# Optimization experiments

Measured on AMD Instinct MI355X. Metric: run time of the kernel, lower is better.

The kernel has to match this reference:

```python
import jax, jax.numpy as jnp
import numpy as np

B, S, D = 4, 1024, 4096
HQ, HKV = 32, 8
HD = D // HQ          # 128
SCALE = HQ // HKV     # 4 (GQA repeat factor)


def setup_inputs() -> dict:
    key = jax.random.key(0)
    ks = jax.random.split(key, 11)
    s = 0.02  # init scale for weights
    return {
        "x": jax.random.normal(ks[0], (B, S, D), jnp.float32),
        # freqs_cis stored as (real, imag) pairs: [S, HD//2, 2]
        "freqs_cis": jax.random.normal(ks[1], (S, HD // 2, 2), jnp.float32),
        "Wq": jax.random.normal(ks[2], (D, HQ * HD), jnp.float32) * s,
        "bq": jnp.zeros((HQ * HD,), jnp.float32),
        "Wk": jax.random.normal(ks[3], (D, HKV * HD), jnp.float32) * s,
        "bk": jnp.zeros((HKV * HD,), jnp.float32),
        "Wv": jax.random.normal(ks[4], (D, HKV * HD), jnp.float32) * s,
        "bv": jnp.zeros((HKV * HD,), jnp.float32),
        "Wo": jax.random.normal(ks[5], (D, D), jnp.float32) * s,
        "bo": jnp.zeros((D,), jnp.float32),
        "startpos": 0,
    }


def _apply_rotary(x, fc):
    # x: [B, S, H, HD]; fc: [S, HD//2, 2] (real, imag)
    xr = x.reshape(*x.shape[:-1], HD // 2, 2)
    a, b = xr[..., 0], xr[..., 1]
    c = fc[None, :, None, :, 0]  # [1, S, 1, HD//2]
    d = fc[None, :, None, :, 1]
    # complex multiply (a+ib)*(c+id)
    out = jnp.stack([a * c - b * d, a * d + b * c], axis=-1)
    return out.reshape(x.shape)


def reference(x, freqs_cis, Wq, bq, Wk, bk, Wv, bv, Wo, bo, startpos):
    b, s, _ = x.shape
    q = (x @ Wq + bq).reshape(b, s, HQ, HD)
    k = (x @ Wk + bk).reshape(b, s, HKV, HD)
    v = (x @ Wv + bv).reshape(b, s, HKV, HD)

    fc = freqs_cis[startpos:startpos + s]
    q = _apply_rotary(q, fc)
    k = _apply_rotary(k, fc)

    # startpos == 0 and seq == cache_seq: cache write/read is identity
    q = q.transpose(0, 2, 1, 3)                            # [b, HQ, s, HD]
    k = jnp.repeat(k.transpose(0, 2, 1, 3), SCALE, axis=1)  # GQA repeat -> [b, HQ, s, HD]
    v = jnp.repeat(v.transpose(0, 2, 1, 3), SCALE, axis=1)

    scores = jnp.einsum('bhqd,bhkd->bhqk', q, k) / jnp.sqrt(jnp.float32(HD))
    causal = jnp.tril(jnp.ones((s, s), bool))
    scores = jnp.where(causal, scores, -jnp.inf)
    attn = jax.nn.softmax(scores, axis=-1)
    o = jnp.einsum('bhqk,bhkd->bhqd', attn, v)
    o = o.transpose(0, 2, 1, 3).reshape(b, s, HQ * HD)
    return o @ Wo + bo
```

## Files before the change

### kernel.cpp

```cpp
#include <hip/hip_runtime.h>
#include <hip/hip_bf16.h>

using bf16x8   = __attribute__((ext_vector_type(8))) __bf16;
using floatx4  = __attribute__((ext_vector_type(4))) float;
using floatx16 = __attribute__((ext_vector_type(16))) float;

#define DEVINL __device__ __forceinline__

DEVINL void gload16(const void* g, void* l) {
  __builtin_amdgcn_global_load_lds(
      (__attribute__((address_space(1))) void*)g,
      (__attribute__((address_space(3))) void*)l,
      16, 0, 0);
}

constexpr int S_ = 1024, D_ = 4096, HQ_ = 32, HKV_ = 8, HD_ = 128, B_ = 4;

__global__ void conv_bf16(const float* __restrict__ in, __bf16* __restrict__ out, int n) {
  int i = (blockIdx.x * 256 + threadIdx.x) * 8;
  if (i >= n) return;
  float4 a = *(const float4*)(in + i);
  float4 b = *(const float4*)(in + i + 4);
  bf16x8 o;
  o[0] = (__bf16)a.x; o[1] = (__bf16)a.y; o[2] = (__bf16)a.z; o[3] = (__bf16)a.w;
  o[4] = (__bf16)b.x; o[5] = (__bf16)b.y; o[6] = (__bf16)b.z; o[7] = (__bf16)b.w;
  *(bf16x8*)(out + i) = o;
}

__global__ void conv_transpose(const float* __restrict__ W, __bf16* __restrict__ WT, int K, int N) {
  __shared__ float tile[32][33];
  int n0 = blockIdx.x * 32, k0 = blockIdx.y * 32;
  int tx = threadIdx.x & 31, ty = threadIdx.x >> 5;
#pragma unroll
  for (int i = 0; i < 32; i += 8)
    tile[ty + i][tx] = W[(size_t)(k0 + ty + i) * N + n0 + tx];
  __syncthreads();
#pragma unroll
  for (int i = 0; i < 32; i += 8)
    WT[(size_t)(n0 + ty + i) * K + k0 + tx] = (__bf16)tile[tx][ty + i];
}

template<int MODE>
__global__ __launch_bounds__(512, 1)
void gemm8p(const __bf16* __restrict__ A, const __bf16* __restrict__ BT,
            const float* __restrict__ b0, const float* __restrict__ b1,
            const float* __restrict__ b2, void* __restrict__ Cout,
            int M, int N, int K)
{
  __shared__ __bf16 lds[65536];
  const int t = threadIdx.x;
  const int lane = t & 63, w = t >> 6;
  const int wm = w >> 2, wn = w & 3;
  const int g = (lane >> 4) & 3, c = lane & 15;

  const int gridX = gridDim.x;
  const int nwg = gridDim.x * gridDim.y;
  int lin = blockIdx.y * gridDim.x + blockIdx.x;
  lin = (lin & 7) * (nwg >> 3) + (lin >> 3);
  const int bx = lin % gridX, by = lin / gridX;
  const int m0 = by * 256, n0 = bx * 256;

  const floatx4 zero4 = {0.f, 0.f, 0.f, 0.f};
  floatx4 acc[2][2][4][2];
#pragma unroll
  for (int a = 0; a < 2; a++)
#pragma unroll
    for (int bq = 0; bq < 2; bq++)
#pragma unroll
      for (int i = 0; i < 4; i++)
#pragma unroll
        for (int j = 0; j < 2; j++) acc[a][bq][i][j] = zero4;

  const int t3 = t >> 3;
  const int l8 = ((t & 7) ^ (t3 & 7)) * 8;
  const int browc = (t3 & 31) + ((t3 >> 5) << 6);
  const __bf16* srcA0 = A  + (size_t)(m0 + t3) * K + l8;
  const __bf16* srcA1 = A  + (size_t)(m0 + 64 + t3) * K + l8;
  const __bf16* srcB0 = BT + (size_t)(n0 + browc) * K + l8;
  const __bf16* srcB1 = BT + (size_t)(n0 + 32 + browc) * K + l8;
  const size_t k128 = (size_t)128 * K;

  const int arow_rd = (wm * 64 + c) * 64;
  const int brow_rd = (wn * 32 + c) * 64;
  const int sel0 = ((g) ^ (c & 7)) * 8;
  const int sel1 = ((4 + g) ^ (c & 7)) * 8;

  const int NT = K >> 6;

  bf16x8 af[4][2], bf0[2][2], bf1[2][2];

#define STG(srcp, subofs, kt, pbuf)                                              \
  gload16((srcp) + (size_t)(kt) * 64,        &lds[(pbuf) + (subofs) + t * 8]);   \
  gload16((srcp) + (size_t)(kt) * 64 + k128, &lds[(pbuf) + (subofs) + 4096 + t * 8]);

#define LOADA(MQ, bb)                                                            \
  _Pragma("unroll")                                                              \
  for (int i = 0; i < 4; i++) {                                                  \
    af[i][0] = *(const bf16x8*)&lds[(bb) + (MQ)*8192 + arow_rd + i*1024 + sel0]; \
    af[i][1] = *(const bf16x8*)&lds[(bb) + (MQ)*8192 + arow_rd + i*1024 + sel1]; \
  }

#define LOADB(DST, NQ, bb)                                                       \
  _Pragma("unroll")                                                              \
  for (int j = 0; j < 2; j++) {                                                  \
    DST[j][0] = *(const bf16x8*)&lds[(bb) + 16384 + (NQ)*8192 + brow_rd + j*1024 + sel0]; \
    DST[j][1] = *(const bf16x8*)&lds[(bb) + 16384 + (NQ)*8192 + brow_rd + j*1024 + sel1]; \
  }

#define MFMAQ(MQ, NQ, BF)                                                        \
  __builtin_amdgcn_s_setprio(1);                                                 \
  _Pragma("unroll")                                                              \
  for (int i = 0; i < 4; i++)                                                    \
    _Pragma("unroll")                                                            \
    for (int j = 0; j < 2; j++) {                                                \
      acc[MQ][NQ][i][j] = __builtin_amdgcn_mfma_f32_16x16x32_bf16(af[i][0], BF[j][0], acc[MQ][NQ][i][j], 0, 0, 0); \
      acc[MQ][NQ][i][j] = __builtin_amdgcn_mfma_f32_16x16x32_bf16(af[i][1], BF[j][1], acc[MQ][NQ][i][j], 0, 0, 0); \
    }                                                                            \
  __builtin_amdgcn_s_setprio(0);

#define SBAR() __builtin_amdgcn_sched_barrier(0)
#define BARR() __builtin_amdgcn_s_barrier()
#define VMC(N) asm volatile("s_waitcnt vmcnt(" #N ")" ::: "memory");
#define LGKM0() asm volatile("s_waitcnt lgkmcnt(0)" ::: "memory");

  STG(srcA0, 0, 0, 0)
  STG(srcB0, 16384, 0, 0)
  STG(srcB1, 24576, 0, 0)
  STG(srcA1, 8192, 0, 0)
  VMC(4) BARR(); SBAR();

  for (int v = 0; v < NT - 1; ++v) {
    const int bb = (v & 1) * 32768;
    const int nb = bb ^ 32768;
    LOADA(0, bb)
    LOADB(bf0, 0, bb)
    STG(srcA0, 0, v + 1, nb)
    SBAR(); VMC(4) BARR(); LGKM0() SBAR();
    MFMAQ(0, 0, bf0)
    SBAR(); BARR(); SBAR();
    LOADB(bf1, 1, bb)
    STG(srcB0, 16384, v + 1, nb)
    SBAR(); VMC(4) BARR(); LGKM0() SBAR();
    MFMAQ(0, 1, bf1)
    SBAR(); BARR(); SBAR();
    LOADA(1, bb)
    STG(srcB1, 24576, v + 1, nb)
    SBAR(); BARR(); LGKM0() SBAR();
    MFMAQ(1, 1, bf1)
    SBAR(); BARR(); SBAR();
    STG(srcA1, 8192, v + 1, nb)
    SBAR(); VMC(4) BARR(); SBAR();
    MFMAQ(1, 0, bf0)
    SBAR(); BARR(); SBAR();
  }
  {
    const int bb = ((NT - 1) & 1) * 32768;
    LOADA(0, bb)
    LOADB(bf0, 0, bb)
    SBAR(); VMC(2) BARR(); LGKM0() SBAR();
    MFMAQ(0, 0, bf0)
    SBAR(); BARR(); SBAR();
    LOADB(bf1, 1, bb)
    SBAR(); VMC(0) BARR(); LGKM0() SBAR();
    MFMAQ(0, 1, bf1)
    SBAR(); BARR(); SBAR();
    LOADA(1, bb)
    SBAR(); BARR(); LGKM0() SBAR();
    MFMAQ(1, 1, bf1)
    MFMAQ(1, 0, bf0)
  }

#undef STG
#undef LOADA
#undef LOADB
#undef MFMAQ
#undef SBAR
#undef BARR
#undef VMC
#undef LGKM0

#pragma unroll
  for (int mq = 0; mq < 2; mq++)
#pragma unroll
    for (int nq = 0; nq < 2; nq++)
#pragma unroll
      for (int j = 0; j < 2; j++) {
        const int ncol = n0 + wn * 64 + nq * 32 + j * 16 + c;
#pragma unroll
        for (int i = 0; i < 4; i++) {
          const int mbase = m0 + wm * 128 + mq * 64 + i * 16 + g * 4;
#pragma unroll
          for (int r = 0; r < 4; r++) {
            const int m = mbase + r;
            float v = acc[mq][nq][i][j][r];
            if constexpr (MODE == 0) {
              ((float*)Cout)[(size_t)m * N + ncol] = v + b0[ncol];
            } else {
              const int bb2 = m >> 10, s = m & 1023;
              __bf16* qkv = (__bf16*)Cout;
              if (ncol < 4096) {
                v += b0[ncol];
                const int h = ncol >> 7, d = ncol & 127;
                qkv[(((size_t)bb2 * 32 + h) * 1024 + s) * 128 + d] = (__bf16)v;
              } else if (ncol < 5120) {
                const int nc = ncol - 4096;
                v += b1[nc];
                const int h = nc >> 7, d = nc & 127;
                qkv[16777216 + (((size_t)bb2 * 8 + h) * 1024 + s) * 128 + d] = (__bf16)v;
              } else {
                const int nc = ncol - 5120;
                v += b2[nc];
                const int h = nc >> 7, d = nc & 127;
                qkv[20971520 + (((size_t)bb2 * 8 + h) * 128 + d) * 1024 + s] = (__bf16)v;
              }
            }
          }
        }
      }
}

constexpr int NQCH = B_ * HQ_ * S_ * (HD_ / 8);
constexpr int NKCH = B_ * HKV_ * S_ * (HD_ / 8);
__global__ void rope_kernel(__bf16* __restrict__ qt, __bf16* __restrict__ kt,
                            const float* __restrict__ fc, const int* __restrict__ sp) {
  int tid = blockIdx.x * 256 + threadIdx.x;
  __bf16* p;
  int idx;
  if (tid < NQCH) { p = qt; idx = tid; }
  else { idx = tid - NQCH; if (idx >= NKCH) return; p = kt; }
  const int c8 = idx & 15;
  const int s  = (idx >> 4) & 1023;
  const int srow = sp[0] + s;
  const float* f = fc + (size_t)srow * 128 + c8 * 8;
  float4 fa = *(const float4*)(f);
  float4 fb = *(const float4*)(f + 4);
  __bf16* q = p + (size_t)idx * 8;
  bf16x8 v = *(const bf16x8*)q;
  float a0 = (float)v[0], b0 = (float)v[1], a1 = (float)v[2], b1 = (float)v[3];
  float a2 = (float)v[4], b2 = (float)v[5], a3 = (float)v[6], b3 = (float)v[7];
  bf16x8 o;
  o[0] = (__bf16)(a0 * fa.x - b0 * fa.y); o[1] = (__bf16)(a0 * fa.y + b0 * fa.x);
  o[2] = (__bf16)(a1 * fa.z - b1 * fa.w); o[3] = (__bf16)(a1 * fa.w + b1 * fa.z);
  o[4] = (__bf16)(a2 * fb.x - b2 * fb.y); o[5] = (__bf16)(a2 * fb.y + b2 * fb.x);
  o[6] = (__bf16)(a3 * fb.z - b3 * fb.w); o[7] = (__bf16)(a3 * fb.w + b3 * fb.z);
  *(bf16x8*)q = o;
}

__global__ __launch_bounds__(256, 2)
void flash_attn(const __bf16* __restrict__ qt, const __bf16* __restrict__ kt,
                const __bf16* __restrict__ vt, __bf16* __restrict__ obuf)
{
  const int lane = threadIdx.x & 63, w = threadIdx.x >> 6;
  const int rl = lane & 31, hi = lane >> 5;
  const int qb = blockIdx.x & 7;
  const int bh = blockIdx.x >> 3;
  const int b = bh >> 5, h = bh & 31, hk = h >> 2;
  const int q0w = (qb + w * 8) * 32;

  const __bf16* Qp = qt + (size_t)(b * HQ_ + h) * S_ * HD_;
  const __bf16* Kp = kt + (size_t)(b * HKV_ + hk) * S_ * HD_;
  const __bf16* Vp = vt + (size_t)(b * HKV_ + hk) * HD_ * S_;

  const __bf16* Qb = Qp + (size_t)(q0w + rl) * HD_ + hi * 8;
  bf16x8 qf[8];
#pragma unroll
  for (int d = 0; d < 8; d++) qf[d] = *(const bf16x8*)(Qb + d * 16);

  const __bf16* Kb = Kp + (size_t)rl * HD_ + hi * 8;
  const __bf16* Vb = Vp + (size_t)rl * S_ + hi * 8;

  const floatx16 zero16 = {0.f,0.f,0.f,0.f,0.f,0.f,0.f,0.f,0.f,0.f,0.f,0.f,0.f,0.f,0.f,0.f};
  floatx16 oacc[4];
#pragma unroll
  for (int dt = 0; dt < 4; dt++) oacc[dt] = zero16;

  float m_run = -__builtin_inff();
  float l_run = 0.f;
  const float ksc = 0.12751744875895f;

  for (int kv0 = 0; kv0 <= q0w; kv0 += 32) {
    floatx16 acc = zero16;
    bf16x8 kf[8];
#pragma unroll
    for (int d = 0; d < 8; d++)
      kf[d] = *(const bf16x8*)(Kb + (size_t)kv0 * HD_ + d * 16);
#pragma unroll
    for (int d = 0; d < 8; d++)
      acc = __builtin_amdgcn_mfma_f32_32x32x16_bf16(kf[d], qf[d], acc, 0, 0, 0);

    bf16x8 vf[4][2];
#pragma unroll
    for (int dt = 0; dt < 4; dt++)
#pragma unroll
      for (int kh = 0; kh < 2; kh++)
        vf[dt][kh] = *(const bf16x8*)(Vb + (size_t)dt * 32 * S_ + kv0 + kh * 16);

    if (kv0 == q0w) {
#pragma unroll
      for (int r = 0; r < 16; r++) {
        const int krel = (r & 3) + 8 * (r >> 2) + 4 * hi;
        if (krel > rl) acc[r] = -3e29f;
      }
    }

    float mx = acc[0];
#pragma unroll
    for (int r = 1; r < 16; r++) mx = fmaxf(mx, acc[r]);
    mx = fmaxf(mx, __shfl_xor(mx, 32));
    const float m_cand = mx * ksc;

    float m_use;
    const bool defer = __all(m_cand - m_run <= 8.0f);
    if (defer) {
      m_use = m_run;
    } else {
      const float m_new = fmaxf(m_run, m_cand);
      const float alpha = exp2f(m_run - m_new);
      l_run *= alpha;
      float ar[16];
#pragma unroll
      for (int r = 0; r < 16; r++)
        ar[r] = __shfl(alpha, (r & 3) + 8 * (r >> 2) + 4 * hi);
#pragma unroll
      for (int dt = 0; dt < 4; dt++)
#pragma unroll
        for (int r = 0; r < 16; r++) oacc[dt][r] *= ar[r];
      m_run = m_new;
      m_use = m_new;
    }

    float pr[16];
#pragma unroll
    for (int r = 0; r < 16; r++) pr[r] = exp2f(fmaf(acc[r], ksc, -m_use));
    float rs = pr[0];
#pragma unroll
    for (int r = 1; r < 16; r++) rs += pr[r];
    rs += __shfl_xor(rs, 32);
    l_run += rs;

    bf16x8 pa[2];
#pragma unroll
    for (int kh = 0; kh < 2; kh++) {
      const int rb = kh * 8;
      unsigned a0, b0, a1, b1;
      asm("v_cvt_pk_bf16_f32 %0, %1, %2" : "=v"(a0) : "v"(pr[rb + 0]), "v"(pr[rb + 1]));
      asm("v_cvt_pk_bf16_f32 %0, %1, %2" : "=v"(b0) : "v"(pr[rb + 4]), "v"(pr[rb + 5]));
      asm("v_cvt_pk_bf16_f32 %0, %1, %2" : "=v"(a1) : "v"(pr[rb + 2]), "v"(pr[rb + 3]));
      asm("v_cvt_pk_bf16_f32 %0, %1, %2" : "=v"(b1) : "v"(pr[rb + 6]), "v"(pr[rb + 7]));
      asm("v_permlane32_swap_b32 %0, %1" : "+v"(a0), "+v"(b0));
      asm("v_permlane32_swap_b32 %0, %1" : "+v"(a1), "+v"(b1));
      union { unsigned u[4]; bf16x8 v; } cvt;
      cvt.u[0] = a0; cvt.u[1] = a1; cvt.u[2] = b0; cvt.u[3] = b1;
      pa[kh] = cvt.v;
    }

#pragma unroll
    for (int dt = 0; dt < 4; dt++) {
      oacc[dt] = __builtin_amdgcn_mfma_f32_32x32x16_bf16(pa[0], vf[dt][0], oacc[dt], 0, 0, 0);
      oacc[dt] = __builtin_amdgcn_mfma_f32_32x32x16_bf16(pa[1], vf[dt][1], oacc[dt], 0, 0, 0);
    }
  }

  const float linv = 1.f / l_run;
  float lr[16];
#pragma unroll
  for (int r = 0; r < 16; r++)
    lr[r] = __shfl(linv, (r & 3) + 8 * (r >> 2) + 4 * hi);
#pragma unroll
  for (int dt = 0; dt < 4; dt++)
#pragma unroll
    for (int r = 0; r < 16; r++) {
      const int qrow = q0w + (r & 3) + 8 * (r >> 2) + 4 * hi;
      const size_t o = (size_t)(b * S_ + qrow) * D_ + h * HD_ + dt * 32 + rl;
      obuf[o] = (__bf16)(oacc[dt][r] * lr[r]);
    }
}

extern "C" void kernel_launch(void* const* d_in, const int* in_sizes, int n_in,
                              void* d_out, int out_size, void* d_ws, size_t ws_size,
                              hipStream_t stream) {
  (void)in_sizes; (void)n_in; (void)out_size;
  const float* x  = (const float*)d_in[0];
  const float* fc = (const float*)d_in[1];
  const float* Wq = (const float*)d_in[2];
  const float* bq = (const float*)d_in[3];
  const float* Wk = (const float*)d_in[4];
  const float* bk = (const float*)d_in[5];
  const float* Wv = (const float*)d_in[6];
  const float* bv = (const float*)d_in[7];
  const float* Wo = (const float*)d_in[8];
  const float* bo = (const float*)d_in[9];
  const int*   sp = (const int*)d_in[10];
  float* out = (float*)d_out;

  const size_t MB = 1024 * 1024;
  if (ws_size < 192 * MB) return;
  char* ws = (char*)d_ws;
  __bf16* xb     = (__bf16*)(ws + 0);
  __bf16* WqkvT  = (__bf16*)(ws + 32 * MB);
  __bf16* WoT    = (__bf16*)(ws + 80 * MB);
  __bf16* q_t    = (__bf16*)(ws + 112 * MB);
  __bf16* k_t    = (__bf16*)(ws + 144 * MB);
  __bf16* v_t    = (__bf16*)(ws + 152 * MB);
  __bf16* ob     = (__bf16*)(ws + 160 * MB);

  conv_bf16<<<8192, 256, 0, stream>>>(x, xb, D_ * B_ * S_);
  conv_transpose<<<dim3(128, 128), 256, 0, stream>>>(Wq, WqkvT, 4096, 4096);
  conv_transpose<<<dim3(32, 128),  256, 0, stream>>>(Wk, WqkvT + (size_t)4096 * 4096, 4096, 1024);
  conv_transpose<<<dim3(32, 128),  256, 0, stream>>>(Wv, WqkvT + (size_t)5120 * 4096, 4096, 1024);
  conv_transpose<<<dim3(128, 128), 256, 0, stream>>>(Wo, WoT, 4096, 4096);

  gemm8p<1><<<dim3(24, 16), 512, 0, stream>>>(xb, WqkvT, bq, bk, bv, q_t, 4096, 6144, 4096);

  rope_kernel<<<(NQCH + NKCH) / 256, 256, 0, stream>>>(q_t, k_t, fc, sp);
  flash_attn<<<1024, 256, 0, stream>>>(q_t, k_t, v_t, ob);

  gemm8p<0><<<dim3(16, 16), 512, 0, stream>>>(ob, WoT, bo, nullptr, nullptr, out, 4096, 4096, 4096);
}
```

Baseline: 613.0 us.

## Replace output-projection GEMM with smaller-tile 128x128 kernel

```diff
diff --git a/kernel.cpp b/kernel.cpp
--- a/kernel.cpp
+++ b/kernel.cpp
@@ -40,12 +40,11 @@
     WT[(size_t)(n0 + ty + i) * K + k0 + tx] = (__bf16)tile[tx][ty + i];
 }
 
-template<int MODE>
 __global__ __launch_bounds__(512, 1)
-void gemm8p(const __bf16* __restrict__ A, const __bf16* __restrict__ BT,
-            const float* __restrict__ b0, const float* __restrict__ b1,
-            const float* __restrict__ b2, void* __restrict__ Cout,
-            int M, int N, int K)
+void gemm8p_qkv(const __bf16* __restrict__ A, const __bf16* __restrict__ BT,
+                const float* __restrict__ b0, const float* __restrict__ b1,
+                const float* __restrict__ b2, void* __restrict__ Cout,
+                int M, int N, int K)
 {
   __shared__ __bf16 lds[65536];
   const int t = threadIdx.x;
@@ -193,30 +192,99 @@
           for (int r = 0; r < 4; r++) {
             const int m = mbase + r;
             float v = acc[mq][nq][i][j][r];
-            if constexpr (MODE == 0) {
-              ((float*)Cout)[(size_t)m * N + ncol] = v + b0[ncol];
+            const int bb2 = m >> 10, s = m & 1023;
+            __bf16* qkv = (__bf16*)Cout;
+            if (ncol < 4096) {
+              v += b0[ncol];
+              const int h = ncol >> 7, d = ncol & 127;
+              qkv[(((size_t)bb2 * 32 + h) * 1024 + s) * 128 + d] = (__bf16)v;
+            } else if (ncol < 5120) {
+              const int nc = ncol - 4096;
+              v += b1[nc];
+              const int h = nc >> 7, d = nc & 127;
+              qkv[16777216 + (((size_t)bb2 * 8 + h) * 1024 + s) * 128 + d] = (__bf16)v;
             } else {
-              const int bb2 = m >> 10, s = m & 1023;
-              __bf16* qkv = (__bf16*)Cout;
-              if (ncol < 4096) {
-                v += b0[ncol];
-                const int h = ncol >> 7, d = ncol & 127;
-                qkv[(((size_t)bb2 * 32 + h) * 1024 + s) * 128 + d] = (__bf16)v;
-              } else if (ncol < 5120) {
-                const int nc = ncol - 4096;
-                v += b1[nc];
-                const int h = nc >> 7, d = nc & 127;
-                qkv[16777216 + (((size_t)bb2 * 8 + h) * 1024 + s) * 128 + d] = (__bf16)v;
-              } else {
-                const int nc = ncol - 5120;
-                v += b2[nc];
-                const int h = nc >> 7, d = nc & 127;
-                qkv[20971520 + (((size_t)bb2 * 8 + h) * 128 + d) * 1024 + s] = (__bf16)v;
-              }
+              const int nc = ncol - 5120;
+              v += b2[nc];
+              const int h = nc >> 7, d = nc & 127;
+              qkv[20971520 + (((size_t)bb2 * 8 + h) * 128 + d) * 1024 + s] = (__bf16)v;
             }
           }
         }
       }
+}
+
+__global__ __launch_bounds__(256, 2)
+void gemm_oproj(const __bf16* __restrict__ A, const __bf16* __restrict__ BT,
+                const float* __restrict__ bias, float* __restrict__ Cout,
+                int M, int N, int K)
+{
+  __shared__ __bf16 Alds[4096];
+  __shared__ __bf16 Blds[4096];
+  const int t = threadIdx.x;
+  const int lane = t & 63;
+  const int w = t >> 6;
+  const int wr = w >> 1, wc = w & 1;
+  const int g = lane >> 4, c = lane & 15;
+
+  const int nwg = gridDim.x * gridDim.y;
+  int lin = blockIdx.y * gridDim.x + blockIdx.x;
+  lin = (lin & 7) * (nwg >> 3) + (lin >> 3);
+  const int bx = lin % gridDim.x, by = lin / gridDim.x;
+  const int m0 = by * 128, n0 = bx * 128;
+
+  const floatx4 zero4 = {0.f, 0.f, 0.f, 0.f};
+  floatx4 acc[4][4];
+#pragma unroll
+  for (int i = 0; i < 4; i++)
+#pragma unroll
+    for (int j = 0; j < 4; j++) acc[i][j] = zero4;
+
+  const int srow = t >> 2;
+  const int ga = (t & 3) ^ ((t >> 3) & 3);
+  const __bf16* Ar = A  + (size_t)(m0 + srow) * K + ga * 8;
+  const __bf16* Br = BT + (size_t)(n0 + srow) * K + ga * 8;
+  const size_t rstep = (size_t)64 * K;
+
+  const int sl = (g ^ ((c >> 1) & 3)) * 8;
+  const int aoff = (wr * 64 + c) * 32 + sl;
+  const int boff = (wc * 64 + c) * 32 + sl;
+
+  for (int kt = 0; kt < K; kt += 32) {
+    gload16(Ar + kt,         &Alds[t * 8]);
+    gload16(Ar + rstep + kt, &Alds[(t + 256) * 8]);
+    gload16(Br + kt,         &Blds[t * 8]);
+    gload16(Br + rstep + kt, &Blds[(t + 256) * 8]);
+    __syncthreads();
+    bf16x8 af[4], bfr[4];
+#pragma unroll
+    for (int i = 0; i < 4; i++)
+      af[i] = *(const bf16x8*)&Alds[aoff + i * 512];
+#pragma unroll
+    for (int j = 0; j < 4; j++)
+      bfr[j] = *(const bf16x8*)&Blds[boff + j * 512];
+#pragma unroll
+    for (int i = 0; i < 4; i++)
+#pragma unroll
+      for (int j = 0; j < 4; j++)
+        acc[i][j] = __builtin_amdgcn_mfma_f32_16x16x32_bf16(af[i], bfr[j], acc[i][j], 0, 0, 0);
+    __syncthreads();
+  }
+
+#pragma unroll
+  for (int j = 0; j < 4; j++) {
+    const int ncol = n0 + wc * 64 + j * 16 + c;
+    const float bv = bias[ncol];
+#pragma unroll
+    for (int i = 0; i < 4; i++) {
+      const int mbase = m0 + wr * 64 + i * 16 + g * 4;
+#pragma unroll
+      for (int r = 0; r < 4; r++) {
+        const int m = mbase + r;
+        Cout[(size_t)m * N + ncol] = acc[i][j][r] + bv;
+      }
+    }
+  }
 }
 
 constexpr int NQCH = B_ * HQ_ * S_ * (HD_ / 8);
@@ -410,10 +478,10 @@
   conv_transpose<<<dim3(32, 128),  256, 0, stream>>>(Wv, WqkvT + (size_t)5120 * 4096, 4096, 1024);
   conv_transpose<<<dim3(128, 128), 256, 0, stream>>>(Wo, WoT, 4096, 4096);
 
-  gemm8p<1><<<dim3(24, 16), 512, 0, stream>>>(xb, WqkvT, bq, bk, bv, q_t, 4096, 6144, 4096);
+  gemm8p_qkv<<<dim3(24, 16), 512, 0, stream>>>(xb, WqkvT, bq, bk, bv, q_t, 4096, 6144, 4096);
 
   rope_kernel<<<(NQCH + NKCH) / 256, 256, 0, stream>>>(q_t, k_t, fc, sp);
   flash_attn<<<1024, 256, 0, stream>>>(q_t, k_t, v_t, ob);
 
-  gemm8p<0><<<dim3(16, 16), 512, 0, stream>>>(ob, WoT, bo, nullptr, nullptr, out, 4096, 4096, 4096);
-}
+  gemm_oproj<<<dim3(32, 32), 256, 0, stream>>>(ob, WoT, bo, out, 4096, 4096, 4096);
+}
```

After: 648.6 us. 1.06x slower.

## Restructure GEMM main loop to stage loads deeper with unrolled double-buffer schedule

Applied to the files above, without the earlier changes.

```diff
diff --git a/kernel.cpp b/kernel.cpp
--- a/kernel.cpp
+++ b/kernel.cpp
@@ -42,10 +42,10 @@
 
 template<int MODE>
 __global__ __launch_bounds__(512, 1)
-void gemm8p(const __bf16* __restrict__ A, const __bf16* __restrict__ BT,
-            const float* __restrict__ b0, const float* __restrict__ b1,
-            const float* __restrict__ b2, void* __restrict__ Cout,
-            int M, int N, int K)
+void gemm8(const __bf16* __restrict__ A, const __bf16* __restrict__ BT,
+           const float* __restrict__ b0, const float* __restrict__ b1,
+           const float* __restrict__ b2, void* __restrict__ Cout,
+           int M, int N, int K)
 {
   __shared__ __bf16 lds[65536];
   const int t = threadIdx.x;
@@ -86,6 +86,7 @@
   const int sel1 = ((4 + g) ^ (c & 7)) * 8;
 
   const int NT = K >> 6;
+  const int NI = NT >> 1;
 
   bf16x8 af[4][2], bf0[2][2], bf1[2][2];
 
@@ -127,44 +128,79 @@
   STG(srcB0, 16384, 0, 0)
   STG(srcB1, 24576, 0, 0)
   STG(srcA1, 8192, 0, 0)
-  VMC(4) BARR(); SBAR();
-
-  for (int v = 0; v < NT - 1; ++v) {
-    const int bb = (v & 1) * 32768;
-    const int nb = bb ^ 32768;
-    LOADA(0, bb)
-    LOADB(bf0, 0, bb)
-    STG(srcA0, 0, v + 1, nb)
-    SBAR(); VMC(4) BARR(); LGKM0() SBAR();
+  STG(srcA0, 0, 1, 32768)
+  STG(srcB0, 16384, 1, 32768)
+  STG(srcB1, 24576, 1, 32768)
+  VMC(6) BARR(); SBAR();
+
+  for (int i = 0; i < NI - 1; ++i) {
+    const int tb = 2 * i + 1, tc = 2 * i + 2, td = 2 * i + 3;
+    LOADA(0, 0) LOADB(bf0, 0, 0)
+    STG(srcA1, 8192, tb, 32768)
+    SBAR(); BARR(); LGKM0() SBAR();
     MFMAQ(0, 0, bf0)
     SBAR(); BARR(); SBAR();
-    LOADB(bf1, 1, bb)
-    STG(srcB0, 16384, v + 1, nb)
-    SBAR(); VMC(4) BARR(); LGKM0() SBAR();
+    LOADB(bf1, 1, 0)
+    STG(srcA0, 0, tc, 0)
+    SBAR(); BARR(); LGKM0() SBAR();
     MFMAQ(0, 1, bf1)
     SBAR(); BARR(); SBAR();
-    LOADA(1, bb)
-    STG(srcB1, 24576, v + 1, nb)
+    LOADA(1, 0)
+    STG(srcB0, 16384, tc, 0)
     SBAR(); BARR(); LGKM0() SBAR();
     MFMAQ(1, 1, bf1)
     SBAR(); BARR(); SBAR();
-    STG(srcA1, 8192, v + 1, nb)
-    SBAR(); VMC(4) BARR(); SBAR();
+    STG(srcB1, 24576, tc, 0)
+    SBAR(); VMC(6) BARR(); SBAR();
+    MFMAQ(1, 0, bf0)
+    SBAR(); BARR(); SBAR();
+    LOADA(0, 32768) LOADB(bf0, 0, 32768)
+    STG(srcA1, 8192, tc, 0)
+    SBAR(); BARR(); LGKM0() SBAR();
+    MFMAQ(0, 0, bf0)
+    SBAR(); BARR(); SBAR();
+    LOADB(bf1, 1, 32768)
+    STG(srcA0, 0, td, 32768)
+    SBAR(); BARR(); LGKM0() SBAR();
+    MFMAQ(0, 1, bf1)
+    SBAR(); BARR(); SBAR();
+    LOADA(1, 32768)
+    STG(srcB0, 16384, td, 32768)
+    SBAR(); BARR(); LGKM0() SBAR();
+    MFMAQ(1, 1, bf1)
+    SBAR(); BARR(); SBAR();
+    STG(srcB1, 24576, td, 32768)
+    SBAR(); VMC(6) BARR(); SBAR();
     MFMAQ(1, 0, bf0)
     SBAR(); BARR(); SBAR();
   }
   {
-    const int bb = ((NT - 1) & 1) * 32768;
-    LOADA(0, bb)
-    LOADB(bf0, 0, bb)
-    SBAR(); VMC(2) BARR(); LGKM0() SBAR();
+    const int tb = NT - 1;
+    LOADA(0, 0) LOADB(bf0, 0, 0)
+    STG(srcA1, 8192, tb, 32768)
+    SBAR(); BARR(); LGKM0() SBAR();
     MFMAQ(0, 0, bf0)
     SBAR(); BARR(); SBAR();
-    LOADB(bf1, 1, bb)
-    SBAR(); VMC(0) BARR(); LGKM0() SBAR();
+    LOADB(bf1, 1, 0)
+    SBAR(); BARR(); LGKM0() SBAR();
     MFMAQ(0, 1, bf1)
     SBAR(); BARR(); SBAR();
-    LOADA(1, bb)
+    LOADA(1, 0)
+    SBAR(); BARR(); LGKM0() SBAR();
+    MFMAQ(1, 1, bf1)
+    SBAR(); BARR(); SBAR();
+    SBAR(); VMC(0) BARR(); SBAR();
+    MFMAQ(1, 0, bf0)
+    SBAR(); BARR(); SBAR();
+    LOADA(0, 32768) LOADB(bf0, 0, 32768)
+    SBAR(); BARR(); LGKM0() SBAR();
+    MFMAQ(0, 0, bf0)
+    SBAR(); BARR(); SBAR();
+    LOADB(bf1, 1, 32768)
+    SBAR(); BARR(); LGKM0() SBAR();
+    MFMAQ(0, 1, bf1)
+    SBAR(); BARR(); SBAR();
+    LOADA(1, 32768)
     SBAR(); BARR(); LGKM0() SBAR();
     MFMAQ(1, 1, bf1)
     MFMAQ(1, 0, bf0)
@@ -410,10 +446,10 @@
   conv_transpose<<<dim3(32, 128),  256, 0, stream>>>(Wv, WqkvT + (size_t)5120 * 4096, 4096, 1024);
   conv_transpose<<<dim3(128, 128), 256, 0, stream>>>(Wo, WoT, 4096, 4096);
 
-  gemm8p<1><<<dim3(24, 16), 512, 0, stream>>>(xb, WqkvT, bq, bk, bv, q_t, 4096, 6144, 4096);
+  gemm8<1><<<dim3(24, 16), 512, 0, stream>>>(xb, WqkvT, bq, bk, bv, q_t, 4096, 6144, 4096);
 
   rope_kernel<<<(NQCH + NKCH) / 256, 256, 0, stream>>>(q_t, k_t, fc, sp);
   flash_attn<<<1024, 256, 0, stream>>>(q_t, k_t, v_t, ob);
 
-  gemm8p<0><<<dim3(16, 16), 512, 0, stream>>>(ob, WoT, bo, nullptr, nullptr, out, 4096, 4096, 4096);
-}
+  gemm8<0><<<dim3(16, 16), 512, 0, stream>>>(ob, WoT, bo, nullptr, nullptr, out, 4096, 4096, 4096);
+}
```

Result: slower. 670.4 us (+9.4%).
